# Optimization experiments

Measured on AMD Instinct MI355X. Metric: run time of the kernel, lower is better.

Reference implementation:

```python
import jax, jax.numpy as jnp
import numpy as np

V, E, DY, DZ, H, B, T = 32000, 100, 200, 500, 700, 32, 128

def _glorot(key, shape):
    fan_in, fan_out = shape[0], shape[-1]
    lim = np.sqrt(6.0 / (fan_in + fan_out)).astype(np.float32)
    return jax.random.uniform(key, shape, jnp.float32, -lim, lim)

def setup_inputs() -> dict:
    key = jax.random.key(0)
    ks = jax.random.split(key, 16)
    labels = jax.random.randint(ks[0], (B,), 0, 2).astype(jnp.float32)
    z = jax.random.normal(ks[1], (B, DZ), jnp.float32)
    dec_inputs = jax.random.randint(ks[2], (B, T), 0, V)
    # tf.nn.dropout(rate=0.5): keep w.p. 0.5, scale kept by 1/0.5 -> mask in {0, 2}
    dropout_mask = (jax.random.uniform(ks[3], (B, T, H)) < 0.5).astype(jnp.float32) * 2.0
    emb = jax.random.normal(ks[4], (V, E), jnp.float32) * 0.05
    W1 = _glorot(ks[5], (1, DY)); b1 = jnp.zeros((DY,), jnp.float32)
    gru1_k = _glorot(ks[6], (E, 3 * H))
    gru1_rk = _glorot(ks[7], (H, 3 * H))
    gru1_b = jnp.zeros((2, 3 * H), jnp.float32)
    proj_W = _glorot(ks[8], (H, V)); proj_b = jnp.zeros((V,), jnp.float32)
    gru3_k = _glorot(ks[9], (E, 3 * H))
    gru3_rk = _glorot(ks[10], (H, 3 * H))
    gru3_b = jnp.zeros((2, 3 * H), jnp.float32)
    return {"labels": labels, "z": z, "dec_inputs": dec_inputs, "dropout_mask": dropout_mask,
            "emb": emb, "W1": W1, "b1": b1,
            "gru1_k": gru1_k, "gru1_rk": gru1_rk, "gru1_b": gru1_b,
            "proj_W": proj_W, "proj_b": proj_b,
            "gru3_k": gru3_k, "gru3_rk": gru3_rk, "gru3_b": gru3_b}

def _run_gru(x_seq, h0, k, rk, b):
    # Keras GRU, reset_after=True: bias shape [2, 3H]
    xp = jnp.einsum('bti,ij->btj', x_seq, k) + b[0]  # input projections for all steps
    def step(h, xp_t):
        hp = h @ rk + b[1]
        xz, xr, xh = jnp.split(xp_t, 3, axis=-1)
        hz, hr, hhp = jnp.split(hp, 3, axis=-1)
        zg = jax.nn.sigmoid(xz + hz)
        rg = jax.nn.sigmoid(xr + hr)
        hh = jnp.tanh(xh + rg * hhp)
        hn = zg * h + (1.0 - zg) * hh
        return hn, hn
    hN, ys = jax.lax.scan(step, h0, jnp.swapaxes(xp, 0, 1))
    return jnp.swapaxes(ys, 0, 1), hN  # [B,T,H], [B,H]

def reference(labels, z, dec_inputs, dropout_mask, emb, W1, b1,
              gru1_k, gru1_rk, gru1_b, proj_W, proj_b,
              gru3_k, gru3_rk, gru3_b):
    x = emb[dec_inputs]                          # [B,T,E]
    lab = labels.reshape(-1, 1)                  # [B,1]
    h_ori = jnp.concatenate([lab @ W1 + b1, z], axis=1)        # [B,H]
    h_tsf = jnp.concatenate([(1.0 - lab) @ W1 + b1, z], axis=1)
    g_outputs, _ = _run_gru(x, h_ori, gru1_k, gru1_rk, gru1_b)  # [B,T,H]
    g = (g_outputs * dropout_mask).reshape(-1, g_outputs.shape[-1])
    g_logits = g @ proj_W + proj_b               # [B*T, V]
    # soft_h_tsf computed in original but unused by the return (pruned by TF/XLA alike)
    _soft, _second = _run_gru(x, h_tsf, gru3_k, gru3_rk, gru3_b)
    return g_logits
```

## Files before the change

kernel.cpp:

```cpp
#include <hip/hip_runtime.h>
#include <hip/hip_bf16.h>

#define B_   32
#define T_   128
#define H_   700
#define E_   100
#define G3   2100
#define V_   32000
#define DY_  200
#define DZ_  500
#define KP   704
#define NBLK 88
#define JW   8
#define FSTR 16
#define BT   4096
#define NTILE (32 * 250)

typedef __attribute__((ext_vector_type(8))) short bf16x8;
typedef __attribute__((ext_vector_type(4))) float f32x4;
typedef __attribute__((ext_vector_type(4))) unsigned u32x4;

__device__ __forceinline__ unsigned ld_flag(const unsigned* p) {
    return __hip_atomic_load(p, __ATOMIC_RELAXED, __HIP_MEMORY_SCOPE_AGENT);
}
__device__ __forceinline__ void st_flag(unsigned* p, unsigned v) {
    __hip_atomic_store(p, v, __ATOMIC_RELAXED, __HIP_MEMORY_SCOPE_AGENT);
}
__device__ __forceinline__ void split_bf(float v, short& hi, short& lo) {
    __hip_bfloat16 h = __float2bfloat16(v);
    float r = v - __bfloat162float(h);
    __hip_bfloat16 l = __float2bfloat16(r);
    hi = *reinterpret_cast<short*>(&h);
    lo = *reinterpret_cast<short*>(&l);
}

#define GLDS16(g, l) __builtin_amdgcn_global_load_lds(                            \
        (const __attribute__((address_space(1))) unsigned int*)(g),               \
        (__attribute__((address_space(3))) unsigned int*)(l), 16, 0, 0)

__global__ __launch_bounds__(256)
void wconv_kernel(const float* __restrict__ W, __hip_bfloat16* __restrict__ Wb) {
    __shared__ float tile[32][33];
    const int n0 = blockIdx.x * 32, k0 = blockIdx.y * 32;
    const int tx = threadIdx.x, ty = threadIdx.y;
    #pragma unroll
    for (int i = 0; i < 4; ++i) {
        int k = k0 + ty + 8 * i;
        float v = (k < H_) ? W[(size_t)k * V_ + n0 + tx] : 0.0f;
        tile[ty + 8 * i][tx] = v;
    }
    __syncthreads();
    #pragma unroll
    for (int i = 0; i < 4; ++i) {
        int nn = ty + 8 * i;
        Wb[(size_t)(n0 + nn) * KP + k0 + tx] = __float2bfloat16(tile[tx][nn]);
    }
}

__global__ __launch_bounds__(256)
void xpt_gemm(const int* __restrict__ di, const float* __restrict__ emb,
              const float* __restrict__ gk, const float* __restrict__ gb,
              float* __restrict__ xpt) {
    __shared__ int di_l[64];
    __shared__ unsigned short Bhi[64][136], Blo[64][136];
    const int tid = threadIdx.x;
    const int c0 = blockIdx.x * 64, n0 = blockIdx.y * 64;
    const int wv = tid >> 6, lane = tid & 63, lr = lane & 15, lkg = lane >> 4;

    if (tid < 64) {
        int tb = n0 + tid;
        di_l[tid] = di[(tb & 31) * T_ + (tb >> 5)];
    }
    __syncthreads();
    for (int e = tid; e < 64 * 128; e += 256) {
        int r = e >> 7, k = e & 127;
        float v = (k < E_) ? emb[(size_t)di_l[r] * E_ + k] : 0.0f;
        short hi, lo; split_bf(v, hi, lo);
        Bhi[r][k] = (unsigned short)hi; Blo[r][k] = (unsigned short)lo;
    }
    __syncthreads();

    bf16x8 ahi[4], alo[4];
    const int crow = c0 + wv * 16 + lr;
    #pragma unroll
    for (int kt = 0; kt < 4; ++kt) {
        #pragma unroll
        for (int i = 0; i < 8; ++i) {
            int k = kt * 32 + lkg * 8 + i;
            float v = (k < E_ && crow < G3) ? gk[(size_t)k * G3 + crow] : 0.0f;
            short hi, lo; split_bf(v, hi, lo);
            ahi[kt][i] = hi; alo[kt][i] = lo;
        }
    }
    f32x4 acc[4];
    #pragma unroll
    for (int n = 0; n < 4; ++n) acc[n] = (f32x4){0.f, 0.f, 0.f, 0.f};
    #pragma unroll
    for (int kt = 0; kt < 4; ++kt) {
        #pragma unroll
        for (int n = 0; n < 4; ++n) {
            bf16x8 bh = *(const bf16x8*)&Bhi[n * 16 + lr][kt * 32 + lkg * 8];
            bf16x8 bl = *(const bf16x8*)&Blo[n * 16 + lr][kt * 32 + lkg * 8];
            acc[n] = __builtin_amdgcn_mfma_f32_16x16x32_bf16(ahi[kt], bh, acc[n], 0, 0, 0);
            acc[n] = __builtin_amdgcn_mfma_f32_16x16x32_bf16(ahi[kt], bl, acc[n], 0, 0, 0);
            acc[n] = __builtin_amdgcn_mfma_f32_16x16x32_bf16(alo[kt], bh, acc[n], 0, 0, 0);
        }
    }
    #pragma unroll
    for (int n = 0; n < 4; ++n)
        #pragma unroll
        for (int r = 0; r < 4; ++r) {
            int cr = c0 + wv * 16 + lkg * 4 + r;
            if (cr < G3)
                xpt[(size_t)cr * BT + n0 + n * 16 + lr] = acc[n][r] + gb[cr];
        }
}

__global__ __launch_bounds__(256, 2)
void mega_kernel(const float* __restrict__ labels, const float* __restrict__ zin,
                 const float* __restrict__ W1, const float* __restrict__ b1,
                 const float* __restrict__ xpt, const float* __restrict__ mask,
                 const float* __restrict__ rk, const float* __restrict__ gb,
                 unsigned short* __restrict__ hb, unsigned short* __restrict__ g_out,
                 unsigned* __restrict__ flags, int* __restrict__ wcnt,
                 const __hip_bfloat16* __restrict__ Bw, const float* __restrict__ bias,
                 float* __restrict__ C) {
    __shared__ float part2[4 * 2 * 16 * 33];
    __shared__ float xbuf[24 * 32];
    __shared__ alignas(16) short smhi[32 * 8], smlo[32 * 8];
    __shared__ alignas(16) unsigned short As[128 * 64];
    __shared__ alignas(16) unsigned short Bs[128 * 64];
    __shared__ int s_idx;

    const int tid = threadIdx.x;
    const int blk = blockIdx.x;

    if (blk < NBLK) {
        const int j0 = blk * JW;
        const int wv = tid >> 6, lane = tid & 63, lr = lane & 15, lkg = lane >> 4;
        const int ktb = (wv < 2) ? wv * 6 : 12 + (wv - 2) * 5;
        const int tn  = (wv < 2) ? 6 : 5;

        bf16x8 bhi[2][6], blo[2][6];
        #pragma unroll
        for (int n = 0; n < 2; ++n)
            #pragma unroll
            for (int t = 0; t < 6; ++t) {
                bf16x8 h8, l8;
                int c = n * 16 + lr;
                int gate = c >> 3, jl = c & 7, j = j0 + jl;
                #pragma unroll
                for (int i = 0; i < 8; ++i) {
                    int k = (ktb + t) * 32 + lkg * 8 + i;
                    float v = (t < tn && c < 24 && j < H_ && k < H_)
                                ? rk[(size_t)k * G3 + gate * H_ + j] : 0.0f;
                    short hi, lo; split_bf(v, hi, lo);
                    h8[i] = hi; l8[i] = lo;
                }
                bhi[n][t] = h8; blo[n][t] = l8;
            }

        const int ob = tid & 31, ojl = tid >> 5, oj = j0 + ojl;
        float hold = 0.f, bz = 0.f, brr = 0.f, bh = 0.f;
        if (oj < H_) {
            bz  = gb[G3 + oj];
            brr = gb[G3 + H_ + oj];
            bh  = gb[G3 + 2 * H_ + oj];
            hold = (oj < DY_) ? labels[ob] * W1[oj] + b1[oj] : zin[ob * DZ_ + (oj - DY_)];
        }
        {
            short hi, lo; split_bf(hold, hi, lo);
            smhi[ob * 8 + ojl] = hi; smlo[ob * 8 + ojl] = lo;
        }
        __syncthreads();
        if (tid < 64) {
            int pl = tid >> 5, q = tid & 31;
            u32x4 d = ((const u32x4*)(pl ? smlo : smhi))[q];
            unsigned short* dst = hb + (size_t)blk * 512 + pl * 256 + q * 8;
            asm volatile("global_store_dwordx4 %0, %1, off sc0 sc1" :: "v"(dst), "v"(d) : "memory");
        }
        asm volatile("s_waitcnt vmcnt(0)" ::: "memory");
        __syncthreads();
        if (tid == 0) st_flag(&flags[blk * FSTR], 1u);

        union FragU { u32x4 u; bf16x8 v; };
        struct Chunk { u32x4 a0, l0, a1, l1; };

#define LOADC(T, C) do {                                                          \
        const unsigned short* rb = hb + (size_t)cur * 45056                       \
                                     + (size_t)((ktb + (T)) * 4 + lkg) * 512;     \
        asm volatile("global_load_dwordx4 %0, %1, off sc0 sc1"                    \
                     : "=v"((C).a0) : "v"(rb + lr * 8) : "memory");               \
        asm volatile("global_load_dwordx4 %0, %1, off sc0 sc1"                    \
                     : "=v"((C).l0) : "v"(rb + 256 + lr * 8) : "memory");         \
        asm volatile("global_load_dwordx4 %0, %1, off sc0 sc1"                    \
                     : "=v"((C).a1) : "v"(rb + 128 + lr * 8) : "memory");         \
        asm volatile("global_load_dwordx4 %0, %1, off sc0 sc1"                    \
                     : "=v"((C).l1) : "v"(rb + 384 + lr * 8) : "memory");         \
    } while (0)
#define PROCC(T, C) do {                                                          \
        FragU fa0, fl0, fa1, fl1;                                                 \
        fa0.u = (C).a0; fl0.u = (C).l0; fa1.u = (C).a1; fl1.u = (C).l1;           \
        _Pragma("unroll")                                                         \
        for (int n = 0; n < 2; ++n) {                                             \
            acc[0][n] = __builtin_amdgcn_mfma_f32_16x16x32_bf16(fa0.v, bhi[n][T], acc[0][n], 0, 0, 0); \
            acc[0][n] = __builtin_amdgcn_mfma_f32_16x16x32_bf16(fa0.v, blo[n][T], acc[0][n], 0, 0, 0); \
            acc[0][n] = __builtin_amdgcn_mfma_f32_16x16x32_bf16(fl0.v, bhi[n][T], acc[0][n], 0, 0, 0); \
            acc[1][n] = __builtin_amdgcn_mfma_f32_16x16x32_bf16(fa1.v, bhi[n][T], acc[1][n], 0, 0, 0); \
            acc[1][n] = __builtin_amdgcn_mfma_f32_16x16x32_bf16(fa1.v, blo[n][T], acc[1][n], 0, 0, 0); \
            acc[1][n] = __builtin_amdgcn_mfma_f32_16x16x32_bf16(fl1.v, bhi[n][T], acc[1][n], 0, 0, 0); \
        }                                                                         \
    } while (0)
#define VWAIT(N) do { asm volatile("s_waitcnt vmcnt(" #N ")" ::: "memory");       \
                      __builtin_amdgcn_sched_barrier(0); } while (0)

        for (int step = 0; step < T_; ++step) {
            const int cur = step & 1, nxt = cur ^ 1;

            #pragma unroll
            for (int it = 0; it < 3; ++it) {
                int e = tid + it * 256;
                int row = e >> 5, b = e & 31;
                int gate = row >> 3, jl = row & 7, j = j0 + jl;
                xbuf[e] = (j < H_) ? xpt[(size_t)(gate * H_ + j) * BT + step * 32 + b] : 0.f;
            }
            float mvr = (oj < H_) ? mask[(size_t)(ob * T_ + step) * H_ + oj] : 0.f;

            if (tid < NBLK) {
                while (ld_flag(&flags[tid * FSTR]) < (unsigned)(step + 1))
                    __builtin_amdgcn_s_sleep(1);
            }
            __syncthreads();
            VWAIT(0);

            f32x4 acc[2][2];
            #pragma unroll
            for (int m = 0; m < 2; ++m)
                #pragma unroll
                for (int n = 0; n < 2; ++n) acc[m][n] = (f32x4){0.f, 0.f, 0.f, 0.f};
            Chunk c0, c1, c2;
            LOADC(0, c0); LOADC(1, c1); LOADC(2, c2);
            VWAIT(8); PROCC(0, c0); LOADC(3, c0);
            VWAIT(8); PROCC(1, c1); LOADC(4, c1);
            VWAIT(8); PROCC(2, c2); LOADC(5, c2);
            VWAIT(8); PROCC(3, c0);
            VWAIT(4); PROCC(4, c1);
            VWAIT(0); PROCC(5, c2);

            #pragma unroll
            for (int m = 0; m < 2; ++m)
                #pragma unroll
                for (int n = 0; n < 2; ++n)
                    #pragma unroll
                    for (int r = 0; r < 4; ++r)
                        part2[((wv * 2 + m) * 16 + lkg * 4 + r) * 33 + n * 16 + lr] = acc[m][n][r];
            __syncthreads();

            {
                int m = ob >> 4, row = ob & 15;
                float hp0 = bz, hp1 = brr, hp2 = bh;
                #pragma unroll
                for (int w = 0; w < 4; ++w) {
                    int base = ((w * 2 + m) * 16 + row) * 33;
                    hp0 += part2[base + ojl];
                    hp1 += part2[base + 8 + ojl];
                    hp2 += part2[base + 16 + ojl];
                }
                float hn = 0.f, outf = 0.f;
                if (oj < H_) {
                    float xz = xbuf[(0 * 8 + ojl) * 32 + ob];
                    float xr = xbuf[(1 * 8 + ojl) * 32 + ob];
                    float xh = xbuf[(2 * 8 + ojl) * 32 + ob];
                    float zg = 1.0f / (1.0f + expf(-(xz + hp0)));
                    float rg = 1.0f / (1.0f + expf(-(xr + hp1)));
                    float hh = tanhf(xh + rg * hp2);
                    hn = zg * hold + (1.0f - zg) * hh;
                    outf = hn * mvr;
                }
                hold = hn;
                __hip_bfloat16 ov = __float2bfloat16(outf);
                unsigned short us = *(unsigned short*)&ov;
                unsigned short* gp = g_out + (size_t)(step * 32 + ob) * KP + oj;
                asm volatile("global_store_short %0, %1, off sc0 sc1"
                             :: "v"(gp), "v"((unsigned)us) : "memory");
                short hi, lo; split_bf(hn, hi, lo);
                smhi[ob * 8 + ojl] = hi; smlo[ob * 8 + ojl] = lo;
            }
            __syncthreads();
            if (tid < 64) {
                int pl = tid >> 5, q = tid & 31;
                u32x4 d = ((const u32x4*)(pl ? smlo : smhi))[q];
                unsigned short* dst = hb + (size_t)nxt * 45056 + (size_t)blk * 512 + pl * 256 + q * 8;
                asm volatile("global_store_dwordx4 %0, %1, off sc0 sc1" :: "v"(dst), "v"(d) : "memory");
            }
            asm volatile("s_waitcnt vmcnt(0)" ::: "memory");
            __syncthreads();
            if (tid == 0) st_flag(&flags[blk * FSTR], (unsigned)(step + 2));
        }
#undef LOADC
#undef PROCC
#undef VWAIT
    }

    {
        const __hip_bfloat16* Ag = (const __hip_bfloat16*)g_out;
        const int lane = tid & 63, w = tid >> 6;
        const int wm = w >> 1, wn = w & 1;
        const int lr = lane & 15, lkg = lane >> 4;
        const int srl = lane >> 3, scol = (lane & 7) * 8;
        for (;;) {
            __syncthreads();
            if (tid == 0)
                s_idx = __hip_atomic_fetch_add(wcnt, 1, __ATOMIC_RELAXED, __HIP_MEMORY_SCOPE_AGENT);
            __syncthreads();
            const int idx = s_idx;
            if (idx >= NTILE) break;
            const int m = idx / 250, bn = idx - m * 250;
            const unsigned want = (unsigned)(4 * m + 5);
            if (tid < NBLK) {
                while (ld_flag(&flags[tid * FSTR]) < want) __builtin_amdgcn_s_sleep(32);
            }
            __syncthreads();
            const int rowbase = m * 128, colbase = bn * 128;

            f32x4 acc[4][4];
            #pragma unroll
            for (int i = 0; i < 4; ++i)
                #pragma unroll
                for (int j = 0; j < 4; ++j) acc[i][j] = (f32x4){0.f, 0.f, 0.f, 0.f};

            for (int kt = 0; kt < 11; ++kt) {
                const int k0 = kt * 64;
                __syncthreads();
                #pragma unroll
                for (int i = 0; i < 4; ++i) {
                    const int r0 = w * 32 + i * 8;
                    GLDS16(&Ag[(size_t)(rowbase + r0 + srl) * KP + k0 + scol], &As[r0 * 64]);
                    GLDS16(&Bw[(size_t)(colbase + r0 + srl) * KP + k0 + scol], &Bs[r0 * 64]);
                }
                __syncthreads();
                #pragma unroll
                for (int ks = 0; ks < 2; ++ks) {
                    bf16x8 af[4], bf[4];
                    #pragma unroll
                    for (int i = 0; i < 4; ++i)
                        af[i] = *(const bf16x8*)&As[(wm * 64 + i * 16 + lr) * 64 + ks * 32 + lkg * 8];
                    #pragma unroll
                    for (int j = 0; j < 4; ++j)
                        bf[j] = *(const bf16x8*)&Bs[(wn * 64 + j * 16 + lr) * 64 + ks * 32 + lkg * 8];
                    #pragma unroll
                    for (int i = 0; i < 4; ++i)
                        #pragma unroll
                        for (int j = 0; j < 4; ++j)
                            acc[i][j] = __builtin_amdgcn_mfma_f32_16x16x32_bf16(af[i], bf[j], acc[i][j], 0, 0, 0);
                }
            }

            float bv[4];
            #pragma unroll
            for (int j = 0; j < 4; ++j) bv[j] = bias[colbase + wn * 64 + j * 16 + lr];
            #pragma unroll
            for (int i = 0; i < 4; ++i) {
                int gr0 = rowbase + wm * 64 + i * 16 + lkg * 4;
                #pragma unroll
                for (int j = 0; j < 4; ++j) {
                    int gcol = colbase + wn * 64 + j * 16 + lr;
                    #pragma unroll
                    for (int r = 0; r < 4; ++r) {
                        int gr = gr0 + r;
                        int orow = (gr & 31) * T_ + (gr >> 5);
                        C[(size_t)orow * V_ + gcol] = acc[i][j][r] + bv[j];
                    }
                }
            }
        }
    }
}

extern "C" void kernel_launch(void* const* d_in, const int* in_sizes, int n_in,
                              void* d_out, int out_size, void* d_ws, size_t ws_size,
                              hipStream_t stream) {
    const float* labels = (const float*)d_in[0];
    const float* z      = (const float*)d_in[1];
    const int*   di     = (const int*)d_in[2];
    const float* mask   = (const float*)d_in[3];
    const float* emb    = (const float*)d_in[4];
    const float* W1     = (const float*)d_in[5];
    const float* b1     = (const float*)d_in[6];
    const float* g1k    = (const float*)d_in[7];
    const float* g1rk   = (const float*)d_in[8];
    const float* g1b    = (const float*)d_in[9];
    const float* pW     = (const float*)d_in[10];
    const float* pb     = (const float*)d_in[11];

    char* ws = (char*)d_ws;
    unsigned short* g     = (unsigned short*)ws;
    __hip_bfloat16* Wb    = (__hip_bfloat16*)(ws + 5767168);
    float*          xpt   = (float*)(ws + 50823168);
    unsigned short* hb    = (unsigned short*)(ws + 85229568);
    unsigned*       flags = (unsigned*)(ws + 85409792);
    int*            wcnt  = (int*)(ws + 85415424);

    hipMemsetAsync(flags, 0, 5632 + 64, stream);

    xpt_gemm<<<dim3(33, 64), 256, 0, stream>>>(di, emb, g1k, g1b, xpt);
    wconv_kernel<<<dim3(1000, 22), dim3(32, 8), 0, stream>>>(pW, Wb);

    mega_kernel<<<dim3(512), 256, 0, stream>>>(labels, z, W1, b1, xpt, mask,
                                               g1rk, g1b, hb, g, flags, wcnt,
                                               Wb, pb, (float*)d_out);
}
```

Baseline: 806.2 us.

## Fold weight conversion into mega kernel and overlap with GRU recurrence

Drops the separate weight-transpose/bf16 conversion kernel. The non-GRU blocks of the persistent mega kernel now do that conversion while the 88 GRU blocks run the recurrence, with a counter barrier placed before the projection GEMM. Blocks grow to 512 threads using dynamic shared memory, so the GRU K-split uses 8 waves instead of 4. GEMM tiles become 128x256 and output stores use non-temporal writes. Risks include fewer resident blocks, a global spin barrier, and each block waiting on conversion before any GEMM tile can start.

```diff
diff --git a/kernel.cpp b/kernel.cpp
--- a/kernel.cpp
+++ b/kernel.cpp
@@ -14,7 +14,8 @@
 #define JW   8
 #define FSTR 16
 #define BT   4096
-#define NTILE (32 * 250)
+#define NWORK 168
+#define NTILE 4000
 
 typedef __attribute__((ext_vector_type(8))) short bf16x8;
 typedef __attribute__((ext_vector_type(4))) float f32x4;
@@ -37,25 +38,6 @@
 #define GLDS16(g, l) __builtin_amdgcn_global_load_lds(                            \
         (const __attribute__((address_space(1))) unsigned int*)(g),               \
         (__attribute__((address_space(3))) unsigned int*)(l), 16, 0, 0)
-
-__global__ __launch_bounds__(256)
-void wconv_kernel(const float* __restrict__ W, __hip_bfloat16* __restrict__ Wb) {
-    __shared__ float tile[32][33];
-    const int n0 = blockIdx.x * 32, k0 = blockIdx.y * 32;
-    const int tx = threadIdx.x, ty = threadIdx.y;
-    #pragma unroll
-    for (int i = 0; i < 4; ++i) {
-        int k = k0 + ty + 8 * i;
-        float v = (k < H_) ? W[(size_t)k * V_ + n0 + tx] : 0.0f;
-        tile[ty + 8 * i][tx] = v;
-    }
-    __syncthreads();
-    #pragma unroll
-    for (int i = 0; i < 4; ++i) {
-        int nn = ty + 8 * i;
-        Wb[(size_t)(n0 + nn) * KP + k0 + tx] = __float2bfloat16(tile[tx][nn]);
-    }
-}
 
 __global__ __launch_bounds__(256)
 void xpt_gemm(const int* __restrict__ di, const float* __restrict__ emb,
@@ -116,20 +98,23 @@
         }
 }
 
-__global__ __launch_bounds__(256, 2)
+__global__ __launch_bounds__(512, 2)
 void mega_kernel(const float* __restrict__ labels, const float* __restrict__ zin,
                  const float* __restrict__ W1, const float* __restrict__ b1,
                  const float* __restrict__ xpt, const float* __restrict__ mask,
                  const float* __restrict__ rk, const float* __restrict__ gb,
                  unsigned short* __restrict__ hb, unsigned short* __restrict__ g_out,
-                 unsigned* __restrict__ flags, int* __restrict__ wcnt,
-                 const __hip_bfloat16* __restrict__ Bw, const float* __restrict__ bias,
-                 float* __restrict__ C) {
-    __shared__ float part2[4 * 2 * 16 * 33];
-    __shared__ float xbuf[24 * 32];
-    __shared__ alignas(16) short smhi[32 * 8], smlo[32 * 8];
-    __shared__ alignas(16) unsigned short As[128 * 64];
-    __shared__ alignas(16) unsigned short Bs[128 * 64];
+                 unsigned* __restrict__ flags, unsigned* __restrict__ ctrs,
+                 const float* __restrict__ W, __hip_bfloat16* __restrict__ Wb,
+                 const float* __restrict__ bias, float* __restrict__ C) {
+    extern __shared__ char dynsm[];
+    unsigned short* As = (unsigned short*)dynsm;
+    unsigned short* Bs = (unsigned short*)(dynsm + 16384);
+    float (*wtile)[33] = (float(*)[33])(dynsm + 49152);
+    float* part2 = (float*)dynsm;
+    float* xbuf  = (float*)(dynsm + 33792);
+    short* smhi  = (short*)(dynsm + 36864);
+    short* smlo  = (short*)(dynsm + 37376);
     __shared__ int s_idx;
 
     const int tid = threadIdx.x;
@@ -138,14 +123,14 @@
     if (blk < NBLK) {
         const int j0 = blk * JW;
         const int wv = tid >> 6, lane = tid & 63, lr = lane & 15, lkg = lane >> 4;
-        const int ktb = (wv < 2) ? wv * 6 : 12 + (wv - 2) * 5;
-        const int tn  = (wv < 2) ? 6 : 5;
-
-        bf16x8 bhi[2][6], blo[2][6];
+        const int ktb = (wv < 6) ? wv * 3 : 18 + (wv - 6) * 2;
+        const int tn  = (wv < 6) ? 3 : 2;
+
+        bf16x8 bhi[2][3], blo[2][3];
         #pragma unroll
         for (int n = 0; n < 2; ++n)
             #pragma unroll
-            for (int t = 0; t < 6; ++t) {
+            for (int t = 0; t < 3; ++t) {
                 bf16x8 h8, l8;
                 int c = n * 16 + lr;
                 int gate = c >> 3, jl = c & 7, j = j0 + jl;
@@ -160,15 +145,15 @@
                 bhi[n][t] = h8; blo[n][t] = l8;
             }
 
-        const int ob = tid & 31, ojl = tid >> 5, oj = j0 + ojl;
+        const int ob = tid & 31, ojl = (tid >> 5) & 7, oj = j0 + ojl;
         float hold = 0.f, bz = 0.f, brr = 0.f, bh = 0.f;
-        if (oj < H_) {
-            bz  = gb[G3 + oj];
-            brr = gb[G3 + H_ + oj];
-            bh  = gb[G3 + 2 * H_ + oj];
-            hold = (oj < DY_) ? labels[ob] * W1[oj] + b1[oj] : zin[ob * DZ_ + (oj - DY_)];
-        }
-        {
+        if (tid < 256) {
+            if (oj < H_) {
+                bz  = gb[G3 + oj];
+                brr = gb[G3 + H_ + oj];
+                bh  = gb[G3 + 2 * H_ + oj];
+                hold = (oj < DY_) ? labels[ob] * W1[oj] + b1[oj] : zin[ob * DZ_ + (oj - DY_)];
+            }
             short hi, lo; split_bf(hold, hi, lo);
             smhi[ob * 8 + ojl] = hi; smlo[ob * 8 + ojl] = lo;
         }
@@ -186,21 +171,21 @@
         union FragU { u32x4 u; bf16x8 v; };
         struct Chunk { u32x4 a0, l0, a1, l1; };
 
-#define LOADC(T, C) do {                                                          \
+#define LOADC(T, Cc) do {                                                         \
         const unsigned short* rb = hb + (size_t)cur * 45056                       \
                                      + (size_t)((ktb + (T)) * 4 + lkg) * 512;     \
         asm volatile("global_load_dwordx4 %0, %1, off sc0 sc1"                    \
-                     : "=v"((C).a0) : "v"(rb + lr * 8) : "memory");               \
+                     : "=v"((Cc).a0) : "v"(rb + lr * 8) : "memory");              \
         asm volatile("global_load_dwordx4 %0, %1, off sc0 sc1"                    \
-                     : "=v"((C).l0) : "v"(rb + 256 + lr * 8) : "memory");         \
+                     : "=v"((Cc).l0) : "v"(rb + 256 + lr * 8) : "memory");        \
         asm volatile("global_load_dwordx4 %0, %1, off sc0 sc1"                    \
-                     : "=v"((C).a1) : "v"(rb + 128 + lr * 8) : "memory");         \
+                     : "=v"((Cc).a1) : "v"(rb + 128 + lr * 8) : "memory");        \
         asm volatile("global_load_dwordx4 %0, %1, off sc0 sc1"                    \
-                     : "=v"((C).l1) : "v"(rb + 384 + lr * 8) : "memory");         \
+                     : "=v"((Cc).l1) : "v"(rb + 384 + lr * 8) : "memory");        \
     } while (0)
-#define PROCC(T, C) do {                                                          \
+#define PROCC(T, Cc) do {                                                         \
         FragU fa0, fl0, fa1, fl1;                                                 \
-        fa0.u = (C).a0; fl0.u = (C).l0; fa1.u = (C).a1; fl1.u = (C).l1;           \
+        fa0.u = (Cc).a0; fl0.u = (Cc).l0; fa1.u = (Cc).a1; fl1.u = (Cc).l1;       \
         _Pragma("unroll")                                                         \
         for (int n = 0; n < 2; ++n) {                                             \
             acc[0][n] = __builtin_amdgcn_mfma_f32_16x16x32_bf16(fa0.v, bhi[n][T], acc[0][n], 0, 0, 0); \
@@ -217,14 +202,21 @@
         for (int step = 0; step < T_; ++step) {
             const int cur = step & 1, nxt = cur ^ 1;
 
-            #pragma unroll
-            for (int it = 0; it < 3; ++it) {
-                int e = tid + it * 256;
-                int row = e >> 5, b = e & 31;
-                int gate = row >> 3, jl = row & 7, j = j0 + jl;
-                xbuf[e] = (j < H_) ? xpt[(size_t)(gate * H_ + j) * BT + step * 32 + b] : 0.f;
-            }
-            float mvr = (oj < H_) ? mask[(size_t)(ob * T_ + step) * H_ + oj] : 0.f;
+            {
+                int e = tid;
+                if (e < 768) {
+                    int row = e >> 5, b = e & 31;
+                    int gate = row >> 3, jl = row & 7, j = j0 + jl;
+                    xbuf[e] = (j < H_) ? xpt[(size_t)(gate * H_ + j) * BT + step * 32 + b] : 0.f;
+                }
+                e = tid + 512;
+                if (e < 768) {
+                    int row = e >> 5, b = e & 31;
+                    int gate = row >> 3, jl = row & 7, j = j0 + jl;
+                    xbuf[e] = (j < H_) ? xpt[(size_t)(gate * H_ + j) * BT + step * 32 + b] : 0.f;
+                }
+            }
+            float mvr = (tid < 256 && oj < H_) ? mask[(size_t)(ob * T_ + step) * H_ + oj] : 0.f;
 
             if (tid < NBLK) {
                 while (ld_flag(&flags[tid * FSTR]) < (unsigned)(step + 1))
@@ -239,13 +231,16 @@
                 #pragma unroll
                 for (int n = 0; n < 2; ++n) acc[m][n] = (f32x4){0.f, 0.f, 0.f, 0.f};
             Chunk c0, c1, c2;
-            LOADC(0, c0); LOADC(1, c1); LOADC(2, c2);
-            VWAIT(8); PROCC(0, c0); LOADC(3, c0);
-            VWAIT(8); PROCC(1, c1); LOADC(4, c1);
-            VWAIT(8); PROCC(2, c2); LOADC(5, c2);
-            VWAIT(8); PROCC(3, c0);
-            VWAIT(4); PROCC(4, c1);
-            VWAIT(0); PROCC(5, c2);
+            if (tn == 3) {
+                LOADC(0, c0); LOADC(1, c1); LOADC(2, c2);
+                VWAIT(8); PROCC(0, c0);
+                VWAIT(4); PROCC(1, c1);
+                VWAIT(0); PROCC(2, c2);
+            } else {
+                LOADC(0, c0); LOADC(1, c1);
+                VWAIT(4); PROCC(0, c0);
+                VWAIT(0); PROCC(1, c1);
+            }
 
             #pragma unroll
             for (int m = 0; m < 2; ++m)
@@ -256,11 +251,11 @@
                         part2[((wv * 2 + m) * 16 + lkg * 4 + r) * 33 + n * 16 + lr] = acc[m][n][r];
             __syncthreads();
 
-            {
+            if (tid < 256) {
                 int m = ob >> 4, row = ob & 15;
                 float hp0 = bz, hp1 = brr, hp2 = bh;
                 #pragma unroll
-                for (int w = 0; w < 4; ++w) {
+                for (int w = 0; w < 8; ++w) {
                     int base = ((w * 2 + m) * 16 + row) * 33;
                     hp0 += part2[base + ojl];
                     hp1 += part2[base + 8 + ojl];
@@ -300,28 +295,66 @@
 #undef LOADC
 #undef PROCC
 #undef VWAIT
-    }
+    } else {
+        const int wi = blk - NBLK;
+        for (int tI = wi; tI < 22000; tI += NWORK) {
+            const int n0 = (tI % 1000) * 32, k0 = (tI / 1000) * 32;
+            if (tid < 256) {
+                int tx = tid & 31, ty = tid >> 5;
+                #pragma unroll
+                for (int i = 0; i < 4; ++i) {
+                    int k = k0 + ty + 8 * i;
+                    wtile[ty + 8 * i][tx] = (k < H_) ? W[(size_t)k * V_ + n0 + tx] : 0.0f;
+                }
+            }
+            __syncthreads();
+            if (tid < 256) {
+                int tx = tid & 31, ty = tid >> 5;
+                #pragma unroll
+                for (int i = 0; i < 4; ++i) {
+                    int nn = ty + 8 * i;
+                    __hip_bfloat16 bv = __float2bfloat16(wtile[tx][nn]);
+                    unsigned short us = *(unsigned short*)&bv;
+                    __hip_bfloat16* wp = Wb + (size_t)(n0 + nn) * KP + k0 + tx;
+                    asm volatile("global_store_short %0, %1, off sc0 sc1"
+                                 :: "v"(wp), "v"((unsigned)us) : "memory");
+                }
+            }
+            __syncthreads();
+        }
+        asm volatile("s_waitcnt vmcnt(0)" ::: "memory");
+        __syncthreads();
+        if (tid == 0)
+            __hip_atomic_fetch_add(&ctrs[FSTR], 1u, __ATOMIC_RELAXED, __HIP_MEMORY_SCOPE_AGENT);
+    }
+
+    if (tid == 0) {
+        while (ld_flag(&ctrs[FSTR]) < (unsigned)NWORK) __builtin_amdgcn_s_sleep(64);
+    }
+    __syncthreads();
 
     {
         const __hip_bfloat16* Ag = (const __hip_bfloat16*)g_out;
+        const __hip_bfloat16* Bw = Wb;
         const int lane = tid & 63, w = tid >> 6;
-        const int wm = w >> 1, wn = w & 1;
+        const int wm = w >> 2, wn = w & 3;
         const int lr = lane & 15, lkg = lane >> 4;
         const int srl = lane >> 3, scol = (lane & 7) * 8;
         for (;;) {
             __syncthreads();
             if (tid == 0)
-                s_idx = __hip_atomic_fetch_add(wcnt, 1, __ATOMIC_RELAXED, __HIP_MEMORY_SCOPE_AGENT);
+                s_idx = (int)__hip_atomic_fetch_add((int*)&ctrs[0], 1, __ATOMIC_RELAXED,
+                                                    __HIP_MEMORY_SCOPE_AGENT);
             __syncthreads();
             const int idx = s_idx;
             if (idx >= NTILE) break;
-            const int m = idx / 250, bn = idx - m * 250;
+            const int m = idx / 125, bn = idx - m * 125;
             const unsigned want = (unsigned)(4 * m + 5);
             if (tid < NBLK) {
-                while (ld_flag(&flags[tid * FSTR]) < want) __builtin_amdgcn_s_sleep(32);
-            }
-            __syncthreads();
-            const int rowbase = m * 128, colbase = bn * 128;
+                while (ld_flag(&flags[tid * FSTR]) < want) __builtin_amdgcn_s_sleep(64);
+            }
+            __syncthreads();
+            const int rowbase = m * 128, colbase = bn * 256;
 
             f32x4 acc[4][4];
             #pragma unroll
@@ -333,9 +366,13 @@
                 const int k0 = kt * 64;
                 __syncthreads();
                 #pragma unroll
+                for (int i = 0; i < 2; ++i) {
+                    const int r0 = w * 16 + i * 8;
+                    GLDS16(&Ag[(size_t)(rowbase + r0 + srl) * KP + k0 + scol], &As[r0 * 64]);
+                }
+                #pragma unroll
                 for (int i = 0; i < 4; ++i) {
                     const int r0 = w * 32 + i * 8;
-                    GLDS16(&Ag[(size_t)(rowbase + r0 + srl) * KP + k0 + scol], &As[r0 * 64]);
                     GLDS16(&Bw[(size_t)(colbase + r0 + srl) * KP + k0 + scol], &Bs[r0 * 64]);
                 }
                 __syncthreads();
@@ -369,7 +406,10 @@
                     for (int r = 0; r < 4; ++r) {
                         int gr = gr0 + r;
                         int orow = (gr & 31) * T_ + (gr >> 5);
-                        C[(size_t)orow * V_ + gcol] = acc[i][j][r] + bv[j];
+                        float val = acc[i][j][r] + bv[j];
+                        float* cp = &C[(size_t)orow * V_ + gcol];
+                        asm volatile("global_store_dword %0, %1, off nt"
+                                     :: "v"(cp), "v"(val) : "memory");
                     }
                 }
             }
@@ -399,14 +439,15 @@
     float*          xpt   = (float*)(ws + 50823168);
     unsigned short* hb    = (unsigned short*)(ws + 85229568);
     unsigned*       flags = (unsigned*)(ws + 85409792);
-    int*            wcnt  = (int*)(ws + 85415424);
+    unsigned*       ctrs  = (unsigned*)(ws + 85415424);
 
     hipMemsetAsync(flags, 0, 5632 + 64, stream);
 
     xpt_gemm<<<dim3(33, 64), 256, 0, stream>>>(di, emb, g1k, g1b, xpt);
-    wconv_kernel<<<dim3(1000, 22), dim3(32, 8), 0, stream>>>(pW, Wb);
-
-    mega_kernel<<<dim3(512), 256, 0, stream>>>(labels, z, W1, b1, xpt, mask,
-                                               g1rk, g1b, hb, g, flags, wcnt,
-                                               Wb, pb, (float*)d_out);
-}
+
+    hipFuncSetAttribute((const void*)mega_kernel,
+                        hipFuncAttributeMaxDynamicSharedMemorySize, 86016);
+    mega_kernel<<<dim3(256), dim3(512), 86016, stream>>>(labels, z, W1, b1, xpt, mask,
+                                                         g1rk, g1b, hb, g, flags, ctrs,
+                                                         pW, Wb, pb, (float*)d_out);
+}
```

New measurement: 1.161 ms. +44.0%, slower.

## Prioritize recurrent GRU blocks, coalesce g_out stores, skip redundant flag polls, nontemporal output stores

Applied to the files above, without the earlier changes.

Recurrent GRU blocks raise their wave priority so that co-resident GEMM work interferes less with the latency-critical serial chain. Per-step g_out bf16 values are staged in shared memory and written as one 16-byte store per batch row instead of scattered 2-byte stores. GEMM tiles skip polling the flags when a previous tile already required an equal or later step, and the poll sleep interval is longer. Logit stores use nontemporal hints to reduce cache pollution from the large output.

```diff
diff --git a/kernel.cpp b/kernel.cpp
--- a/kernel.cpp
+++ b/kernel.cpp
@@ -127,7 +127,7 @@
                  float* __restrict__ C) {
     __shared__ float part2[4 * 2 * 16 * 33];
     __shared__ float xbuf[24 * 32];
-    __shared__ alignas(16) short smhi[32 * 8], smlo[32 * 8];
+    __shared__ alignas(16) short smhi[32 * 8], smlo[32 * 8], smg[32 * 8];
     __shared__ alignas(16) unsigned short As[128 * 64];
     __shared__ alignas(16) unsigned short Bs[128 * 64];
     __shared__ int s_idx;
@@ -136,6 +136,7 @@
     const int blk = blockIdx.x;
 
     if (blk < NBLK) {
+        __builtin_amdgcn_s_setprio(1);
         const int j0 = blk * JW;
         const int wv = tid >> 6, lane = tid & 63, lr = lane & 15, lkg = lane >> 4;
         const int ktb = (wv < 2) ? wv * 6 : 12 + (wv - 2) * 5;
@@ -186,21 +187,21 @@
         union FragU { u32x4 u; bf16x8 v; };
         struct Chunk { u32x4 a0, l0, a1, l1; };
 
-#define LOADC(T, C) do {                                                          \
+#define LOADC(T, Cc) do {                                                         \
         const unsigned short* rb = hb + (size_t)cur * 45056                       \
                                      + (size_t)((ktb + (T)) * 4 + lkg) * 512;     \
         asm volatile("global_load_dwordx4 %0, %1, off sc0 sc1"                    \
-                     : "=v"((C).a0) : "v"(rb + lr * 8) : "memory");               \
+                     : "=v"((Cc).a0) : "v"(rb + lr * 8) : "memory");              \
         asm volatile("global_load_dwordx4 %0, %1, off sc0 sc1"                    \
-                     : "=v"((C).l0) : "v"(rb + 256 + lr * 8) : "memory");         \
+                     : "=v"((Cc).l0) : "v"(rb + 256 + lr * 8) : "memory");        \
         asm volatile("global_load_dwordx4 %0, %1, off sc0 sc1"                    \
-                     : "=v"((C).a1) : "v"(rb + 128 + lr * 8) : "memory");         \
+                     : "=v"((Cc).a1) : "v"(rb + 128 + lr * 8) : "memory");        \
         asm volatile("global_load_dwordx4 %0, %1, off sc0 sc1"                    \
-                     : "=v"((C).l1) : "v"(rb + 384 + lr * 8) : "memory");         \
+                     : "=v"((Cc).l1) : "v"(rb + 384 + lr * 8) : "memory");        \
     } while (0)
-#define PROCC(T, C) do {                                                          \
+#define PROCC(T, Cc) do {                                                         \
         FragU fa0, fl0, fa1, fl1;                                                 \
-        fa0.u = (C).a0; fl0.u = (C).l0; fa1.u = (C).a1; fl1.u = (C).l1;           \
+        fa0.u = (Cc).a0; fl0.u = (Cc).l0; fa1.u = (Cc).a1; fl1.u = (Cc).l1;       \
         _Pragma("unroll")                                                         \
         for (int n = 0; n < 2; ++n) {                                             \
             acc[0][n] = __builtin_amdgcn_mfma_f32_16x16x32_bf16(fa0.v, bhi[n][T], acc[0][n], 0, 0, 0); \
@@ -279,10 +280,7 @@
                 }
                 hold = hn;
                 __hip_bfloat16 ov = __float2bfloat16(outf);
-                unsigned short us = *(unsigned short*)&ov;
-                unsigned short* gp = g_out + (size_t)(step * 32 + ob) * KP + oj;
-                asm volatile("global_store_short %0, %1, off sc0 sc1"
-                             :: "v"(gp), "v"((unsigned)us) : "memory");
+                smg[ob * 8 + ojl] = *(short*)&ov;
                 short hi, lo; split_bf(hn, hi, lo);
                 smhi[ob * 8 + ojl] = hi; smlo[ob * 8 + ojl] = lo;
             }
@@ -292,11 +290,17 @@
                 u32x4 d = ((const u32x4*)(pl ? smlo : smhi))[q];
                 unsigned short* dst = hb + (size_t)nxt * 45056 + (size_t)blk * 512 + pl * 256 + q * 8;
                 asm volatile("global_store_dwordx4 %0, %1, off sc0 sc1" :: "v"(dst), "v"(d) : "memory");
+            } else if (tid < 96) {
+                int b = tid - 64;
+                u32x4 d = ((const u32x4*)smg)[b];
+                unsigned short* gp = g_out + (size_t)(step * 32 + b) * KP + j0;
+                asm volatile("global_store_dwordx4 %0, %1, off sc0 sc1" :: "v"(gp), "v"(d) : "memory");
             }
             asm volatile("s_waitcnt vmcnt(0)" ::: "memory");
             __syncthreads();
             if (tid == 0) st_flag(&flags[blk * FSTR], (unsigned)(step + 2));
         }
+        __builtin_amdgcn_s_setprio(0);
 #undef LOADC
 #undef PROCC
 #undef VWAIT
@@ -308,6 +312,7 @@
         const int wm = w >> 1, wn = w & 1;
         const int lr = lane & 15, lkg = lane >> 4;
         const int srl = lane >> 3, scol = (lane & 7) * 8;
+        unsigned satisfied = 0;
         for (;;) {
             __syncthreads();
             if (tid == 0)
@@ -317,8 +322,11 @@
             if (idx >= NTILE) break;
             const int m = idx / 250, bn = idx - m * 250;
             const unsigned want = (unsigned)(4 * m + 5);
-            if (tid < NBLK) {
-                while (ld_flag(&flags[tid * FSTR]) < want) __builtin_amdgcn_s_sleep(32);
+            if (want > satisfied) {
+                if (tid < NBLK) {
+                    while (ld_flag(&flags[tid * FSTR]) < want) __builtin_amdgcn_s_sleep(64);
+                }
+                satisfied = want;
             }
             __syncthreads();
             const int rowbase = m * 128, colbase = bn * 128;
@@ -369,7 +377,10 @@
                     for (int r = 0; r < 4; ++r) {
                         int gr = gr0 + r;
                         int orow = (gr & 31) * T_ + (gr >> 5);
-                        C[(size_t)orow * V_ + gcol] = acc[i][j][r] + bv[j];
+                        float val = acc[i][j][r] + bv[j];
+                        float* cp = &C[(size_t)orow * V_ + gcol];
+                        asm volatile("global_store_dword %0, %1, off nt"
+                                     :: "v"(cp), "v"(val) : "memory");
                     }
                 }
             }
```

Result: faster. 668.4 us (median of 2 runs) (-17.1%).
